# Kernel tuning notes

Hardware: AMD Instinct MI355X
Metric: run time of the kernel (lower is better)

The kernel has to match this reference:

```python
import jax, jax.numpy as jnp
import numpy as np

DIMENSIONS = 10000
NUM_LEVELS = 100
SIZE = 617
NUM_CLASSES = 26
BATCH = 32


def setup_inputs() -> dict:
    key = jax.random.key(0)
    k1, k2, k3 = jax.random.split(key, 3)
    x = jax.random.uniform(k1, (BATCH, SIZE), dtype=jnp.float32)  # values in [0,1]
    # Random embedding: bipolar {-1,+1} hypervectors
    id_weight = jnp.where(jax.random.uniform(k2, (SIZE, DIMENSIONS)) > 0.5, 1.0, -1.0).astype(jnp.float32)
    # Level embedding: bipolar hypervectors per quantization level
    level_weight = jnp.where(jax.random.uniform(k3, (NUM_LEVELS, DIMENSIONS)) > 0.5, 1.0, -1.0).astype(jnp.float32)
    classify_weight = jnp.zeros((NUM_CLASSES, DIMENSIONS), dtype=jnp.float32)
    return {"x": x, "id_weight": id_weight, "level_weight": level_weight, "classify_weight": classify_weight}


def reference(x, id_weight, level_weight, classify_weight):
    # Level embedding: map continuous values in [low=0, high=1] to level indices
    idx = jnp.clip(jnp.round(x * (NUM_LEVELS - 1)), 0, NUM_LEVELS - 1).astype(jnp.int32)  # (B, S)
    value_hv = level_weight[idx]                     # gather -> (B, S, D)
    bound = id_weight[None, :, :] * value_hv         # bind (elementwise multiply)
    multiset = jnp.sum(bound, axis=1)                # sum over feature axis -> (B, D)
    enc = jnp.where(multiset > 0, 1.0, -1.0)         # hard_quantize
    logit = jnp.einsum('bd,cd->bc', enc, classify_weight)  # Linear, no bias
    return logit
```

## Files before the change

### kernel.cpp

```cpp
#include <hip/hip_runtime.h>

typedef unsigned int u32;
typedef unsigned char u8;
typedef unsigned long long u64;

#define DIMS   10000
#define LEVELS 100
#define SSIZE  617
#define SPAD   624
#define NCLS   26
#define BATCH  32
#define WORDS  313
#define WPITCH 320
#define DPITCH 10240
#define NTILE  5
#define NCH    13
#define CHUNK  48
#define SOPITCH 640

#define OFF_OFFT 0x000000u
#define OFF_IDB  0x020000u
#define OFF_LVB  0x100000u
#define OFF_P8   0x140000u
#define SLOT_BYTES ((size_t)BATCH * DPITCH)

#define PK_ROWS (SPAD + LEVELS + 1)

__global__ __launch_bounds__(256) void k_pack(const float* __restrict__ x,
                                              const float* __restrict__ idw,
                                              const float* __restrict__ lvw,
                                              u32* __restrict__ idb,
                                              u32* __restrict__ lvb,
                                              u32* __restrict__ offt,
                                              float* __restrict__ out)
{
    const int g = blockIdx.x;
    const int r = blockIdx.y;
    const int t = threadIdx.x;
    const bool isLvl = r >= SPAD;
    const int rl = r - SPAD;
    const int d0 = g * 1024 + 4 * t;

    u32 nib = 0;
    const bool rowValid = isLvl ? (rl < LEVELS) : (r < SSIZE);
    if (d0 + 3 < DIMS && rowValid) {
        const float* src = isLvl ? (lvw + (size_t)rl * DIMS)
                                 : (idw + (size_t)r * DIMS);
        float4 f = *(const float4*)(src + d0);
        nib =  (__builtin_bit_cast(u32, f.x) >> 31)
            | ((__builtin_bit_cast(u32, f.y) >> 31) << 1)
            | ((__builtin_bit_cast(u32, f.z) >> 31) << 2)
            | ((__builtin_bit_cast(u32, f.w) >> 31) << 3);
    }
    __shared__ u32 nibs[256];
    nibs[t] = nib;
    __syncthreads();
    if (t < 32) {
        u32 w = 0;
#pragma unroll
        for (int j = 0; j < 8; ++j) w |= nibs[t * 8 + j] << (4 * j);
        u32* dst = isLvl ? (lvb + (size_t)rl * WPITCH)
                         : (idb + (size_t)r * WPITCH);
        dst[g * 32 + t] = w;
    }

    const int B = r * 10 + g;
    const int t2 = B * 256 + t;
    if (t2 < SPAD * BATCH) {
        int s = t2 >> 5, b = t2 & 31;
        u32 off = (u32)LEVELS * WPITCH;
        if (s < SSIZE) {
            float v = x[b * SSIZE + s];
            float rr = rintf(v * (float)(LEVELS - 1));
            int q = (int)rr;
            q = q < 0 ? 0 : (q > LEVELS - 1 ? LEVELS - 1 : q);
            off = (u32)q * WPITCH;
        }
        offt[b * SOPITCH + s] = off;
    }
    if (t2 < BATCH * NCLS) out[t2] = 0.0f;
}

#define CSA6(xv)                                                              \
    {                                                                         \
        u32 car = ones & (xv);                                                \
        ones ^= (xv);                                                         \
        u32 tt;                                                               \
        tt = c0 & car; c0 ^= car; car = tt;                                   \
        tt = c1 & car; c1 ^= car; car = tt;                                   \
        tt = c2 & car; c2 ^= car; car = tt;                                   \
        tt = c3 & car; c3 ^= car; car = tt;                                   \
        c4 ^= car;                                                            \
    }

__device__ __forceinline__ void spread6_1(u32* __restrict__ part,
                                          int slot, int b, int wq,
                                          u32 ones, u32 c0, u32 c1,
                                          u32 c2, u32 c3, u32 c4)
{
    u32* dst = part + ((size_t)(slot * BATCH + b) * DPITCH + (size_t)wq * 32) / 4;
    u32 o[8];
#pragma unroll
    for (int g = 0; g < 8; ++g) {
        int sh = 4 * g;
        u32 n;
        n  =  (((ones >> sh) & 0xFu) * 0x00204081u) & 0x01010101u;
        n |= ((((c0   >> sh) & 0xFu) * 0x00204081u) & 0x01010101u) << 1;
        n |= ((((c1   >> sh) & 0xFu) * 0x00204081u) & 0x01010101u) << 2;
        n |= ((((c2   >> sh) & 0xFu) * 0x00204081u) & 0x01010101u) << 3;
        n |= ((((c3   >> sh) & 0xFu) * 0x00204081u) & 0x01010101u) << 4;
        n |= ((((c4   >> sh) & 0xFu) * 0x00204081u) & 0x01010101u) << 5;
        o[g] = n;
    }
    *(uint4*)(dst)     = make_uint4(o[0], o[1], o[2], o[3]);
    *(uint4*)(dst + 4) = make_uint4(o[4], o[5], o[6], o[7]);
}

template <int CH>
__global__ __launch_bounds__(64) void k_bind_t(const u32* __restrict__ idb,
                                               const u32* __restrict__ lvb,
                                               const u32* __restrict__ offt,
                                               u32* __restrict__ part)
{
    const int wq   = blockIdx.x * 64 + threadIdx.x;
    const int b    = blockIdx.y;
    const int slot = blockIdx.z;
    const int sBeg = slot * CH;

    u32 off[CH];
#pragma unroll
    for (int k = 0; k < CH; ++k) off[k] = offt[b * SOPITCH + sBeg + k];

    u32 ones = 0, c0 = 0, c1 = 0, c2 = 0, c3 = 0, c4 = 0;

#pragma unroll
    for (int grp = 0; grp < CH / 16; ++grp) {
        u32 u[16], l[16];
#pragma unroll
        for (int k = 0; k < 16; ++k) {
            const int s = sBeg + grp * 16 + k;
            u[k] = idb[(size_t)s * WPITCH + wq];
            l[k] = lvb[off[grp * 16 + k] + wq];
        }
#pragma unroll
        for (int k = 0; k < 16; ++k) {
            u32 xv = u[k] ^ l[k];
            CSA6(xv);
        }
    }
    spread6_1(part, slot, b, wq, ones, c0, c1, c2, c3, c4);
}

__global__ __launch_bounds__(64) void k_bind_g(const u32* __restrict__ idb,
                                               const u32* __restrict__ lvb,
                                               const u32* __restrict__ offt,
                                               u32* __restrict__ part,
                                               int chunk)
{
    const int wq   = blockIdx.x * 64 + threadIdx.x;
    const int b    = blockIdx.y;
    const int slot = blockIdx.z;
    const int sBeg = slot * chunk;
    const int sEnd = min(SPAD, sBeg + chunk);

    u32 ones = 0, c0 = 0, c1 = 0, c2 = 0, c3 = 0, c4 = 0;
    for (int s = sBeg; s < sEnd; ++s) {
        u32 u1 = idb[(size_t)s * WPITCH + wq];
        u32 l1 = lvb[offt[b * SOPITCH + s] + wq];
        u32 xv = u1 ^ l1;
        CSA6(xv);
    }
    spread6_1(part, slot, b, wq, ones, c0, c1, c2, c3, c4);
}

template <int NCHT>
__global__ __launch_bounds__(256) void k_encl_t(const u32* __restrict__ part,
                                                const float* __restrict__ W,
                                                float* __restrict__ out)
{
    const int b = blockIdx.y;
    const int q = blockIdx.x;
    const int t = threadIdx.x;
    const int dw = q * 256 + t;
    const u32* p = part + (size_t)b * (DPITCH / 4) + dw;
    const size_t cs = (size_t)BATCH * (DPITCH / 4);

    u32 v[NCHT];
#pragma unroll
    for (int c = 0; c < NCHT; ++c) v[c] = p[(size_t)c * cs];
    u32 a01 = 0, a23 = 0;
#pragma unroll
    for (int c = 0; c < NCHT; ++c) {
        a01 += v[c] & 0x00FF00FFu;
        a23 += (v[c] >> 8) & 0x00FF00FFu;
    }
    const float e0 = (int)(a01 & 0xFFFFu) <= 308 ? 1.0f : -1.0f;
    const float e1 = (int)(a23 & 0xFFFFu) <= 308 ? 1.0f : -1.0f;
    const float e2 = (int)(a01 >> 16)     <= 308 ? 1.0f : -1.0f;
    const float e3 = (int)(a23 >> 16)     <= 308 ? 1.0f : -1.0f;

    float acc[NCLS];
    if (dw < DIMS / 4) {
#pragma unroll
        for (int cc = 0; cc < NCLS; ++cc) {
            float4 w4 = *(const float4*)(W + (size_t)cc * DIMS + 4 * dw);
            acc[cc] = fmaf(e0, w4.x, fmaf(e1, w4.y, fmaf(e2, w4.z, e3 * w4.w)));
        }
    } else {
#pragma unroll
        for (int cc = 0; cc < NCLS; ++cc) acc[cc] = 0.0f;
    }

#pragma unroll
    for (int cc = 0; cc < NCLS; ++cc) {
#pragma unroll
        for (int o = 32; o > 0; o >>= 1)
            acc[cc] += __shfl_xor(acc[cc], o);
    }
    __shared__ float red[4][NCLS];
    const int lane = t & 63, wv = t >> 6;
    if (lane == 0) {
#pragma unroll
        for (int cc = 0; cc < NCLS; ++cc) red[wv][cc] = acc[cc];
    }
    __syncthreads();
    if (t < NCLS) {
        float vv = red[0][t] + red[1][t] + red[2][t] + red[3][t];
        atomicAdd(out + b * NCLS + t, vv);
    }
}

__global__ __launch_bounds__(256) void k_encl_g(const u32* __restrict__ part,
                                                const float* __restrict__ W,
                                                float* __restrict__ out,
                                                int nch)
{
    const int b = blockIdx.y;
    const int q = blockIdx.x;
    const int t = threadIdx.x;
    const int dw = q * 256 + t;
    const u32* p = part + (size_t)b * (DPITCH / 4) + dw;
    const size_t cs = (size_t)BATCH * (DPITCH / 4);
    u32 a01 = 0, a23 = 0;
    for (int c = 0; c < nch; ++c) {
        u32 v = p[(size_t)c * cs];
        a01 += v & 0x00FF00FFu;
        a23 += (v >> 8) & 0x00FF00FFu;
    }
    const float e0 = (int)(a01 & 0xFFFFu) <= 308 ? 1.0f : -1.0f;
    const float e1 = (int)(a23 & 0xFFFFu) <= 308 ? 1.0f : -1.0f;
    const float e2 = (int)(a01 >> 16)     <= 308 ? 1.0f : -1.0f;
    const float e3 = (int)(a23 >> 16)     <= 308 ? 1.0f : -1.0f;
    float acc[NCLS];
    if (dw < DIMS / 4) {
#pragma unroll
        for (int cc = 0; cc < NCLS; ++cc) {
            float4 w4 = *(const float4*)(W + (size_t)cc * DIMS + 4 * dw);
            acc[cc] = fmaf(e0, w4.x, fmaf(e1, w4.y, fmaf(e2, w4.z, e3 * w4.w)));
        }
    } else {
#pragma unroll
        for (int cc = 0; cc < NCLS; ++cc) acc[cc] = 0.0f;
    }
#pragma unroll
    for (int cc = 0; cc < NCLS; ++cc) {
#pragma unroll
        for (int o = 32; o > 0; o >>= 1)
            acc[cc] += __shfl_xor(acc[cc], o);
    }
    __shared__ float red[4][NCLS];
    const int lane = t & 63, wv = t >> 6;
    if (lane == 0) {
#pragma unroll
        for (int cc = 0; cc < NCLS; ++cc) red[wv][cc] = acc[cc];
    }
    __syncthreads();
    if (t < NCLS) {
        float vv = red[0][t] + red[1][t] + red[2][t] + red[3][t];
        atomicAdd(out + b * NCLS + t, vv);
    }
}

extern "C" void kernel_launch(void* const* d_in, const int* in_sizes, int n_in,
                              void* d_out, int out_size, void* d_ws, size_t ws_size,
                              hipStream_t stream)
{
    const float* x   = (const float*)d_in[0];
    const float* idw = (const float*)d_in[1];
    const float* lvw = (const float*)d_in[2];
    const float* W   = (const float*)d_in[3];
    float* out = (float*)d_out;

    char* ws = (char*)d_ws;
    u32* offt = (u32*)(ws + OFF_OFFT);
    u32* idb  = (u32*)(ws + OFF_IDB);
    u32* lvb  = (u32*)(ws + OFF_LVB);
    u32* part = (u32*)(ws + OFF_P8);

    size_t avail = ws_size > OFF_P8 ? ws_size - OFF_P8 : 0;
    const bool fast = avail >= (size_t)NCH * SLOT_BYTES;

    dim3 g1(10, PK_ROWS);
    k_pack<<<g1, 256, 0, stream>>>(x, idw, lvw, idb, lvb, offt, out);

    if (fast) {
        dim3 g2(NTILE, BATCH, NCH);
        k_bind_t<CHUNK><<<g2, 64, 0, stream>>>(idb, lvb, offt, part);
        dim3 g3(10, BATCH);
        k_encl_t<NCH><<<g3, 256, 0, stream>>>(part, W, out);
    } else {
        int nch = (int)(avail / SLOT_BYTES);
        if (nch < 1) nch = 1;
        int chunk = (SPAD + nch - 1) / nch;
        if (chunk > 62) chunk = 62;
        nch = (SPAD + chunk - 1) / chunk;
        dim3 g2(NTILE, BATCH, nch);
        k_bind_g<<<g2, 64, 0, stream>>>(idb, lvb, offt, part, chunk);
        dim3 g3(10, BATCH);
        k_encl_g<<<g3, 256, 0, stream>>>(part, W, out, nch);
    }
}
```

Baseline: 91.31 us.

## Stage level bit-table in LDS and transpose id bits for vector loads

The bind kernel now uses 256-thread blocks covering four batch rows. Each block first stages the 101×64-word slice of the packed level table into shared memory, so level lookups hit LDS instead of global memory. The packed id table is stored transposed (word-major, feature-minor), which lets each thread fetch its feature chunk with 16-byte vector loads. The offset table now stores raw level indices. The cost is that the pack kernel's id writes become strided, and occupancy is limited by the roughly 26 KB of LDS per block.

```diff
diff --git a/kernel.cpp b/kernel.cpp
--- a/kernel.cpp
+++ b/kernel.cpp
@@ -12,6 +12,7 @@
 #define BATCH  32
 #define WORDS  313
 #define WPITCH 320
+#define IDPITCH 640
 #define DPITCH 10240
 #define NTILE  5
 #define NCH    13
@@ -29,7 +30,7 @@
 __global__ __launch_bounds__(256) void k_pack(const float* __restrict__ x,
                                               const float* __restrict__ idw,
                                               const float* __restrict__ lvw,
-                                              u32* __restrict__ idb,
+                                              u32* __restrict__ idb_t,
                                               u32* __restrict__ lvb,
                                               u32* __restrict__ offt,
                                               float* __restrict__ out)
@@ -59,24 +60,24 @@
         u32 w = 0;
 #pragma unroll
         for (int j = 0; j < 8; ++j) w |= nibs[t * 8 + j] << (4 * j);
-        u32* dst = isLvl ? (lvb + (size_t)rl * WPITCH)
-                         : (idb + (size_t)r * WPITCH);
-        dst[g * 32 + t] = w;
+        const int word = g * 32 + t;
+        if (isLvl) lvb[(size_t)rl * WPITCH + word] = w;
+        else       idb_t[(size_t)word * IDPITCH + r] = w;
     }
 
     const int B = r * 10 + g;
     const int t2 = B * 256 + t;
     if (t2 < SPAD * BATCH) {
         int s = t2 >> 5, b = t2 & 31;
-        u32 off = (u32)LEVELS * WPITCH;
+        u32 q = LEVELS;
         if (s < SSIZE) {
             float v = x[b * SSIZE + s];
             float rr = rintf(v * (float)(LEVELS - 1));
-            int q = (int)rr;
-            q = q < 0 ? 0 : (q > LEVELS - 1 ? LEVELS - 1 : q);
-            off = (u32)q * WPITCH;
+            int qi = (int)rr;
+            qi = qi < 0 ? 0 : (qi > LEVELS - 1 ? LEVELS - 1 : qi);
+            q = (u32)qi;
         }
-        offt[b * SOPITCH + s] = off;
+        offt[b * SOPITCH + s] = q;
     }
     if (t2 < BATCH * NCLS) out[t2] = 0.0f;
 }
@@ -117,13 +118,31 @@
 }
 
 template <int CH>
-__global__ __launch_bounds__(64) void k_bind_t(const u32* __restrict__ idb,
-                                               const u32* __restrict__ lvb,
-                                               const u32* __restrict__ offt,
-                                               u32* __restrict__ part)
-{
-    const int wq   = blockIdx.x * 64 + threadIdx.x;
-    const int b    = blockIdx.y;
+__global__ __launch_bounds__(256) void k_bind_t(const u32* __restrict__ idb_t,
+                                                const u32* __restrict__ lvb,
+                                                const u32* __restrict__ offt,
+                                                u32* __restrict__ part)
+{
+    __shared__ u32 tile[(LEVELS + 1) * 64];
+    const int tid = threadIdx.x;
+    const int W0 = blockIdx.x * 64;
+
+    {
+        u32 stg[25];
+#pragma unroll
+        for (int k = 0; k < 25; ++k) {
+            int idx = k * 256 + tid;
+            stg[k] = lvb[(size_t)(idx >> 6) * WPITCH + W0 + (idx & 63)];
+        }
+#pragma unroll
+        for (int k = 0; k < 25; ++k) tile[k * 256 + tid] = stg[k];
+        if (tid < 64) tile[6400 + tid] = 0;
+    }
+    __syncthreads();
+
+    const int lane = tid & 63;
+    const int wq = W0 + lane;
+    const int b = __builtin_amdgcn_readfirstlane(blockIdx.y * 4 + (tid >> 6));
     const int slot = blockIdx.z;
     const int sBeg = slot * CH;
 
@@ -131,27 +150,22 @@
 #pragma unroll
     for (int k = 0; k < CH; ++k) off[k] = offt[b * SOPITCH + sBeg + k];
 
+    alignas(16) u32 idv[CH];
+    const u32* rowp = idb_t + (size_t)wq * IDPITCH + sBeg;
+#pragma unroll
+    for (int k = 0; k < CH / 4; ++k)
+        *(uint4*)&idv[4 * k] = *(const uint4*)(rowp + 4 * k);
+
     u32 ones = 0, c0 = 0, c1 = 0, c2 = 0, c3 = 0, c4 = 0;
-
-#pragma unroll
-    for (int grp = 0; grp < CH / 16; ++grp) {
-        u32 u[16], l[16];
-#pragma unroll
-        for (int k = 0; k < 16; ++k) {
-            const int s = sBeg + grp * 16 + k;
-            u[k] = idb[(size_t)s * WPITCH + wq];
-            l[k] = lvb[off[grp * 16 + k] + wq];
-        }
-#pragma unroll
-        for (int k = 0; k < 16; ++k) {
-            u32 xv = u[k] ^ l[k];
-            CSA6(xv);
-        }
+#pragma unroll
+    for (int k = 0; k < CH; ++k) {
+        u32 xv = idv[k] ^ tile[off[k] * 64 + lane];
+        CSA6(xv);
     }
     spread6_1(part, slot, b, wq, ones, c0, c1, c2, c3, c4);
 }
 
-__global__ __launch_bounds__(64) void k_bind_g(const u32* __restrict__ idb,
+__global__ __launch_bounds__(64) void k_bind_g(const u32* __restrict__ idb_t,
                                                const u32* __restrict__ lvb,
                                                const u32* __restrict__ offt,
                                                u32* __restrict__ part,
@@ -165,8 +179,8 @@
 
     u32 ones = 0, c0 = 0, c1 = 0, c2 = 0, c3 = 0, c4 = 0;
     for (int s = sBeg; s < sEnd; ++s) {
-        u32 u1 = idb[(size_t)s * WPITCH + wq];
-        u32 l1 = lvb[offt[b * SOPITCH + s] + wq];
+        u32 u1 = idb_t[(size_t)wq * IDPITCH + s];
+        u32 l1 = lvb[(size_t)offt[b * SOPITCH + s] * WPITCH + wq];
         u32 xv = u1 ^ l1;
         CSA6(xv);
     }
@@ -292,20 +306,20 @@
     float* out = (float*)d_out;
 
     char* ws = (char*)d_ws;
-    u32* offt = (u32*)(ws + OFF_OFFT);
-    u32* idb  = (u32*)(ws + OFF_IDB);
-    u32* lvb  = (u32*)(ws + OFF_LVB);
-    u32* part = (u32*)(ws + OFF_P8);
+    u32* offt  = (u32*)(ws + OFF_OFFT);
+    u32* idb_t = (u32*)(ws + OFF_IDB);
+    u32* lvb   = (u32*)(ws + OFF_LVB);
+    u32* part  = (u32*)(ws + OFF_P8);
 
     size_t avail = ws_size > OFF_P8 ? ws_size - OFF_P8 : 0;
     const bool fast = avail >= (size_t)NCH * SLOT_BYTES;
 
     dim3 g1(10, PK_ROWS);
-    k_pack<<<g1, 256, 0, stream>>>(x, idw, lvw, idb, lvb, offt, out);
+    k_pack<<<g1, 256, 0, stream>>>(x, idw, lvw, idb_t, lvb, offt, out);
 
     if (fast) {
-        dim3 g2(NTILE, BATCH, NCH);
-        k_bind_t<CHUNK><<<g2, 64, 0, stream>>>(idb, lvb, offt, part);
+        dim3 g2(NTILE, 8, NCH);
+        k_bind_t<CHUNK><<<g2, 256, 0, stream>>>(idb_t, lvb, offt, part);
         dim3 g3(10, BATCH);
         k_encl_t<NCH><<<g3, 256, 0, stream>>>(part, W, out);
     } else {
@@ -315,7 +329,7 @@
         if (chunk > 62) chunk = 62;
         nch = (SPAD + chunk - 1) / chunk;
         dim3 g2(NTILE, BATCH, nch);
-        k_bind_g<<<g2, 64, 0, stream>>>(idb, lvb, offt, part, chunk);
+        k_bind_g<<<g2, 64, 0, stream>>>(idb_t, lvb, offt, part, chunk);
         dim3 g3(10, BATCH);
         k_encl_g<<<g3, 256, 0, stream>>>(part, W, out, nch);
     }
```

New measurement: 93.30 us. +2.2%, slower.
